# Optimization experiments

Measured on AMD Instinct MI355X. Metric: run time of the kernel, lower is better.

The kernel has to match this reference:

```python
import jax, jax.numpy as jnp
import numpy as np

T, C, H, E, TOPK = 8192, 1024, 4096, 8, 2
ALPHA = 0.01


def setup_inputs() -> dict:
    key = jax.random.key(0)
    ks = jax.random.split(key, 10)
    std = 0.01
    return {
        "x": jax.random.normal(ks[0], (T, C), dtype=jnp.float32),
        "gate_w": jax.random.normal(ks[1], (E, C), dtype=jnp.float32) * std,  # nn.init.normal_(std=0.01)
        "wg": jax.random.normal(ks[2], (E, C, H), dtype=jnp.float32) * 0.02,
        "wu": jax.random.normal(ks[3], (E, C, H), dtype=jnp.float32) * 0.02,
        "wd": jax.random.normal(ks[4], (E, H, C), dtype=jnp.float32) * 0.02,
        "swg": jax.random.normal(ks[5], (C, H), dtype=jnp.float32) * 0.02,
        "swu": jax.random.normal(ks[6], (C, H), dtype=jnp.float32) * 0.02,
        "swd": jax.random.normal(ks[7], (H, C), dtype=jnp.float32) * 0.02,
        "shared_scale": jnp.ones((1,), dtype=jnp.float32) * 0.5,
    }


def _swiglu(h, g, u, d):
    # SwiGLU FFN: W_down( silu(W_gate x) * W_up x )
    return (jax.nn.silu(h @ g) * (h @ u)) @ d


def reference(x, gate_w, wg, wu, wd, swg, swu, swd, shared_scale):
    # ---- gate (top-k softmax routing) ----
    logits = x @ gate_w.T                       # [T, E]
    scores = jax.nn.softmax(logits, axis=-1)    # [T, E]
    topk_w, topk_idx = jax.lax.top_k(scores, TOPK)
    topk_w = topk_w / jnp.sum(topk_w, axis=-1, keepdims=True)

    # per-token combine weight for each expert: sum_k w_k * [idx_k == e]  -> [T, E]
    comb = jnp.zeros((x.shape[0], E), dtype=x.dtype)
    comb = comb.at[jnp.arange(x.shape[0])[:, None], topk_idx].add(topk_w)

    # ---- routed experts (dispatch-FFN-combine, expressed as masked dense combine) ----
    y = jnp.zeros_like(x)
    for e in range(E):  # fixed small expert count
        y = y + comb[:, e:e + 1] * _swiglu(x, wg[e], wu[e], wd[e])

    # ---- shared expert ----
    y = y + shared_scale * _swiglu(x, swg, swu, swd)

    # ---- load-balancing aux loss (training mode) ----
    onehot = jax.nn.one_hot(topk_idx.reshape(-1), E, dtype=x.dtype)  # [T*K, E]
    ce = onehot.mean(axis=0)
    fi = ce * E
    Pi = scores.mean(axis=0)
    aux_loss = jnp.sum(Pi * fi) * ALPHA
    return y, aux_loss
```

## Files before the change

kernel.cpp:

```cpp
#include <hip/hip_runtime.h>
#include <hip/hip_bf16.h>
#include <stdint.h>

#define T_TOK 8192
#define CDIM  1024
#define HDIM  4096
#define NEXP  8
#define TOPK_ 2
#define GT_MAX 72
#define UT_MAX 104
#define GROWS_MAX (GT_MAX * 256)

typedef __attribute__((ext_vector_type(8))) short short8;
typedef __attribute__((ext_vector_type(4))) float f32x4;

__device__ __forceinline__ void gload16(const short* g, short* l) {
  __builtin_amdgcn_global_load_lds(
      (const __attribute__((address_space(1))) unsigned int*)(g),
      (__attribute__((address_space(3))) unsigned int*)(l), 16, 0, 0);
}

__global__ __launch_bounds__(256) void gate_kernel(
    const float* __restrict__ x, const float* __restrict__ gw,
    int* __restrict__ tokinfo, float* __restrict__ tokw,
    int* __restrict__ bcnt, float* __restrict__ spart,
    __hip_bfloat16* __restrict__ xb)
{
  const int wid = threadIdx.x >> 6, lane = threadIdx.x & 63;
  const int t = blockIdx.x * 4 + wid;
  float acc[NEXP];
#pragma unroll
  for (int e = 0; e < NEXP; ++e) acc[e] = 0.f;
  const float4* xr = (const float4*)x + (size_t)t * (CDIM / 4);
  const float4* gw4 = (const float4*)gw;
  uint2* xbo = (uint2*)(xb + (size_t)t * CDIM);
#pragma unroll
  for (int i = 0; i < CDIM / 256; ++i) {
    const float4 xv = xr[lane + 64 * i];
    union { __hip_bfloat16 h[4]; uint2 u; } o;
    o.h[0] = __float2bfloat16(xv.x); o.h[1] = __float2bfloat16(xv.y);
    o.h[2] = __float2bfloat16(xv.z); o.h[3] = __float2bfloat16(xv.w);
    xbo[lane + 64 * i] = o.u;
#pragma unroll
    for (int e = 0; e < NEXP; ++e) {
      const float4 gv = gw4[e * (CDIM / 4) + lane + 64 * i];
      acc[e] += xv.x * gv.x + xv.y * gv.y + xv.z * gv.z + xv.w * gv.w;
    }
  }
#pragma unroll
  for (int off = 32; off > 0; off >>= 1) {
#pragma unroll
    for (int e = 0; e < NEXP; ++e) acc[e] += __shfl_xor(acc[e], off);
  }
  float mx = acc[0];
#pragma unroll
  for (int e = 1; e < NEXP; ++e) mx = fmaxf(mx, acc[e]);
  float p[NEXP]; float s = 0.f;
#pragma unroll
  for (int e = 0; e < NEXP; ++e) { p[e] = __expf(acc[e] - mx); s += p[e]; }
  const float inv = 1.f / s;
#pragma unroll
  for (int e = 0; e < NEXP; ++e) p[e] *= inv;
  float v0 = p[0]; int i0 = 0;
#pragma unroll
  for (int e = 1; e < NEXP; ++e) if (p[e] > v0) { v0 = p[e]; i0 = e; }
  float v1 = -1.f; int i1 = 0;
#pragma unroll
  for (int e = 0; e < NEXP; ++e) if (e != i0 && p[e] > v1) { v1 = p[e]; i1 = e; }

  __shared__ float sp[4][NEXP];
  __shared__ int   se[4][2];
  __shared__ float swt[4][2];
  if (lane == 0) {
#pragma unroll
    for (int e = 0; e < NEXP; ++e) sp[wid][e] = p[e];
    const float wn = 1.f / (v0 + v1);
    se[wid][0] = i0; se[wid][1] = i1;
    swt[wid][0] = v0 * wn; swt[wid][1] = v1 * wn;
  }
  __syncthreads();
  if (threadIdx.x == 0) {
    int cnt[NEXP];
#pragma unroll
    for (int e = 0; e < NEXP; ++e) cnt[e] = 0;
#pragma unroll
    for (int tt = 0; tt < 4; ++tt) {
      const int e0 = se[tt][0], e1 = se[tt][1];
      const int r0 = cnt[e0]++; const int r1 = cnt[e1]++;
      tokinfo[blockIdx.x * 4 + tt] = e0 | (e1 << 3) | (r0 << 6) | (r1 << 10);
      ((float2*)tokw)[blockIdx.x * 4 + tt] = make_float2(swt[tt][0], swt[tt][1]);
    }
#pragma unroll
    for (int e = 0; e < NEXP; ++e) bcnt[blockIdx.x * NEXP + e] = cnt[e];
  }
  if (threadIdx.x < NEXP)
    spart[blockIdx.x * NEXP + threadIdx.x] =
        sp[0][threadIdx.x] + sp[1][threadIdx.x] + sp[2][threadIdx.x] + sp[3][threadIdx.x];
}

__global__ __launch_bounds__(512) void scan_kernel(
    const int* __restrict__ bcnt, int* __restrict__ boff, int* __restrict__ ecnt,
    const float* __restrict__ spart, float* __restrict__ aux_out,
    int* __restrict__ pad_off, int* __restrict__ tile_map, int* __restrict__ ntiles)
{
  const int w = threadIdx.x >> 6, l = threadIdx.x & 63;
  int run = 0;
#pragma unroll 4
  for (int c = 0; c < (T_TOK / 4) / 64; ++c) {
    const int b = c * 64 + l;
    const int v = bcnt[b * NEXP + w];
    int sc = v;
#pragma unroll
    for (int off = 1; off < 64; off <<= 1) {
      const int t = __shfl_up(sc, off);
      if (l >= off) sc += t;
    }
    boff[b * NEXP + w] = run + sc - v;
    run += __shfl(sc, 63);
  }
  if (l == 0) ecnt[w] = run;
  float fs = 0.f;
  for (int c = 0; c < (T_TOK / 4) / 64; ++c) fs += spart[(c * 64 + l) * NEXP + w];
#pragma unroll
  for (int off = 32; off > 0; off >>= 1) fs += __shfl_xor(fs, off);
  __shared__ float pis[NEXP];
  __shared__ int cs[NEXP];
  if (l == 0) { pis[w] = fs; cs[w] = run; }
  __syncthreads();
  if (threadIdx.x == 0) {
    float aux = 0.f;
#pragma unroll
    for (int e = 0; e < NEXP; ++e) {
      const float Pi = pis[e] / (float)T_TOK;
      const float ce = (float)cs[e] / (float)(T_TOK * TOPK_);
      aux += Pi * ce * (float)NEXP;
    }
    aux_out[0] = aux * 0.01f;
    ecnt[8] = T_TOK;
    int acc = 0, nt = 0;
    for (int e = 0; e < NEXP; ++e) {
      pad_off[e] = acc;
      const int te = (cs[e] + 255) >> 8;
      for (int t = 0; t < te; ++t) { tile_map[nt] = e | ((t * 256) << 4); ++nt; }
      acc += te * 256;
    }
    ntiles[0] = nt;
    for (int t = 0; t < T_TOK / 256; ++t) { tile_map[nt] = 8 | ((t * 256) << 4); ++nt; }
    ntiles[1] = nt;
  }
}

__global__ __launch_bounds__(256) void scatter_kernel(
    const int* __restrict__ tokinfo, const float* __restrict__ tokw,
    const int* __restrict__ boff, const int* __restrict__ pad_off,
    int* __restrict__ grows, float* __restrict__ gww, int2* __restrict__ tokpos)
{
  const int t = blockIdx.x * 256 + threadIdx.x;
  const int info = tokinfo[t];
  const int e0 = info & 7, e1 = (info >> 3) & 7;
  const int r0 = (info >> 6) & 15, r1 = (info >> 10) & 15;
  const int b = t >> 2;
  const float2 wv = ((const float2*)tokw)[t];
  const int g0 = pad_off[e0] + boff[b * NEXP + e0] + r0;
  grows[g0] = t; gww[g0] = wv.x;
  const int g1 = pad_off[e1] + boff[b * NEXP + e1] + r1;
  grows[g1] = t; gww[g1] = wv.y;
  tokpos[t] = make_int2(g0, g1);
}

struct TD { const float* src; __hip_bfloat16* dst; int N; int nsh; int M; };
struct TB { TD d[27]; };
__global__ __launch_bounds__(256) void tbatch_kernel(TB tb)
{
  const int m = blockIdx.x >> 12;
  const int t = blockIdx.x & 4095;
  const TD td = tb.d[m];
  const int n0 = (t & ((1 << td.nsh) - 1)) << 5;
  const int m0 = (t >> td.nsh) << 5;
  __shared__ float tile[32][33];
  const int tx = threadIdx.x & 31, ty = threadIdx.x >> 5;
#pragma unroll
  for (int i = 0; i < 4; ++i)
    tile[ty + 8 * i][tx] = td.src[(size_t)(m0 + ty + 8 * i) * td.N + n0 + tx];
  __syncthreads();
#pragma unroll
  for (int i = 0; i < 4; ++i)
    td.dst[(size_t)(n0 + ty + 8 * i) * td.M + m0 + tx] = __float2bfloat16(tile[tx][ty + 8 * i]);
}

__global__ __launch_bounds__(512, 2) void gemm1_pipe_kernel(
    const __hip_bfloat16* __restrict__ Abase,
    const __hip_bfloat16* __restrict__ B0mat, const __hip_bfloat16* __restrict__ B1mat,
    __hip_bfloat16* __restrict__ midout,
    const int* __restrict__ rowlist, const int* __restrict__ ecnt,
    const int* __restrict__ tile_map, const int* __restrict__ ntiles,
    int mode, int tile_base)
{
  constexpr int K = CDIM;
  constexpr int NTL = K / 64;
  __shared__ __align__(16) short lds[65536];

  int ti = blockIdx.y + tile_base;
  if (mode == 2) ti += ntiles[0];
  const int hi = (mode == 1) ? ntiles[0] : ntiles[1];
  if (ti >= hi) return;
  const int tm = tile_map[ti];
  const int e = tm & 15, rb = tm >> 4;
  const int rows_valid = ecnt[e] - rb;
  const int gbmid = (int)blockIdx.y * 256;
  const int glist = ti * 256;

  const int t = threadIdx.x, l = t & 63, w = t >> 6;
  const int wr = w >> 2, wc = w & 3;
  const int n0h = blockIdx.x * 128;

  const int rbase = w * 8 + (l >> 3);
  const int ksrc = ((l & 7) ^ ((l >> 3) & 7)) * 8;
  const short* pA[4]; const short* pB[4];
#pragma unroll
  for (int j = 0; j < 4; ++j) {
    const int rl_ = j * 64 + rbase;
    int rg;
    if (e == 8) rg = rb + rl_;
    else { const int c = rl_ < rows_valid ? rl_ : rows_valid - 1; rg = rowlist[glist + c]; }
    pA[j] = (const short*)Abase + (size_t)rg * K + ksrc;
    const int s = (rl_ >> 4) & 1;
    const int h = n0h + (rl_ >> 5) * 16 + (rl_ & 15);
    pB[j] = (const short*)(s ? B1mat : B0mat) + (size_t)e * CDIM * HDIM + (size_t)h * K + ksrc;
  }
  const int dst0 = w * 512 + l * 8;

#define STG(tt) { const int bb_ = ((tt) & 1) * 16384; \
    gload16(pA[0] + (tt) * 64, lds + bb_ + dst0);          gload16(pB[0] + (tt) * 64, lds + 32768 + bb_ + dst0); \
    gload16(pA[1] + (tt) * 64, lds + bb_ + 4096 + dst0);   gload16(pB[1] + (tt) * 64, lds + 32768 + bb_ + 4096 + dst0); \
    gload16(pA[2] + (tt) * 64, lds + bb_ + 8192 + dst0);   gload16(pB[2] + (tt) * 64, lds + 32768 + bb_ + 8192 + dst0); \
    gload16(pA[3] + (tt) * 64, lds + bb_ + 12288 + dst0);  gload16(pB[3] + (tt) * 64, lds + 32768 + bb_ + 12288 + dst0); }

  f32x4 acc[8][4];
#pragma unroll
  for (int i = 0; i < 8; ++i)
#pragma unroll
    for (int j = 0; j < 4; ++j) acc[i][j] = (f32x4){0.f, 0.f, 0.f, 0.f};

  STG(0)
  for (int tt = 0; tt < NTL; ++tt) {
    asm volatile("s_waitcnt vmcnt(0)\n\ts_barrier" ::: "memory");
    __builtin_amdgcn_sched_barrier(0);
    if (tt + 1 < NTL) STG(tt + 1)
    const int ab = (tt & 1) * 16384, bb = 32768 + (tt & 1) * 16384;
#pragma unroll
    for (int ks = 0; ks < 2; ++ks) {
      short8 af[8], bf[4];
      const int cb = ks * 4 + (l >> 4);
      const int csw = (cb ^ (l & 7)) * 8;
#pragma unroll
      for (int mi = 0; mi < 8; ++mi)
        af[mi] = *(const short8*)(lds + ab + (wr * 128 + mi * 16 + (l & 15)) * 64 + csw);
#pragma unroll
      for (int ni = 0; ni < 4; ++ni)
        bf[ni] = *(const short8*)(lds + bb + (wc * 64 + ni * 16 + (l & 15)) * 64 + csw);
      __builtin_amdgcn_s_setprio(1);
#pragma unroll
      for (int mi = 0; mi < 8; ++mi)
#pragma unroll
        for (int ni = 0; ni < 4; ++ni)
          acc[mi][ni] = __builtin_amdgcn_mfma_f32_16x16x32_bf16(af[mi], bf[ni], acc[mi][ni], 0, 0, 0);
      __builtin_amdgcn_s_setprio(0);
    }
  }
#undef STG

  const int rl = (l >> 4) * 4, cl = l & 15;
#pragma unroll
  for (int mi = 0; mi < 8; ++mi) {
#pragma unroll
    for (int j = 0; j < 4; ++j) {
      const int rlocal = wr * 128 + mi * 16 + rl + j;
      if (rlocal < rows_valid) {
        __hip_bfloat16* mp = midout + (size_t)(gbmid + rlocal) * HDIM;
#pragma unroll
        for (int jj = 0; jj < 2; ++jj) {
          const float g = acc[mi][jj * 2][j], u = acc[mi][jj * 2 + 1][j];
          const float sv = g / (1.f + __expf(-g));
          mp[n0h + (wc * 2 + jj) * 16 + cl] = __float2bfloat16(sv * u);
        }
      }
    }
  }
}

template <int OST>
__global__ __launch_bounds__(512, 2) void gemm2_pipe_kernel(
    const __hip_bfloat16* __restrict__ mid, const __hip_bfloat16* __restrict__ wd9,
    float* __restrict__ mid2, float* __restrict__ y,
    const int* __restrict__ rowlist, const float* __restrict__ roww,
    const int* __restrict__ ecnt, const int* __restrict__ tile_map,
    const int* __restrict__ ntiles, const float* __restrict__ ssc,
    int mode, int tile_base)
{
  constexpr int K = HDIM;
  constexpr int NTL = K / 64;
  __shared__ __align__(16) short lds[49152];

  int ti = blockIdx.y + tile_base;
  if (mode == 2) ti += ntiles[0];
  const int hi = (mode == 1) ? ntiles[0] : ntiles[1];
  if (ti >= hi) return;
  const int tm = tile_map[ti];
  const int e = tm & 15, rb = tm >> 4;
  const int rows_valid = ecnt[e] - rb;
  const int gbmid = (int)blockIdx.y * 256;
  const int glist = ti * 256;

  const int t = threadIdx.x, l = t & 63, w = t >> 6;
  const int wr = w & 3, wc = w >> 2;
  const int n0 = blockIdx.x * 128;

  const int rbase = w * 8 + (l >> 3);
  const int ksrc = ((l & 7) ^ ((l >> 3) & 7)) * 8;
  const short* pA[4]; const short* pB[2];
#pragma unroll
  for (int j = 0; j < 4; ++j)
    pA[j] = (const short*)mid + (size_t)(gbmid + j * 64 + rbase) * K + ksrc;
#pragma unroll
  for (int j = 0; j < 2; ++j)
    pB[j] = (const short*)wd9 + (size_t)e * CDIM * HDIM + (size_t)(n0 + j * 64 + rbase) * K + ksrc;
  const int dst0 = w * 512 + l * 8;

#define STG2(tt) { const int ab_ = ((tt) & 1) * 16384, bb_ = 32768 + ((tt) & 1) * 8192; \
    gload16(pA[0] + (size_t)(tt) * 64, lds + ab_ + dst0); \
    gload16(pA[1] + (size_t)(tt) * 64, lds + ab_ + 4096 + dst0); \
    gload16(pA[2] + (size_t)(tt) * 64, lds + ab_ + 8192 + dst0); \
    gload16(pA[3] + (size_t)(tt) * 64, lds + ab_ + 12288 + dst0); \
    gload16(pB[0] + (size_t)(tt) * 64, lds + bb_ + dst0); \
    gload16(pB[1] + (size_t)(tt) * 64, lds + bb_ + 4096 + dst0); }

  f32x4 acc[4][4];
#pragma unroll
  for (int i = 0; i < 4; ++i)
#pragma unroll
    for (int j = 0; j < 4; ++j) acc[i][j] = (f32x4){0.f, 0.f, 0.f, 0.f};

  STG2(0)
  for (int tt = 0; tt < NTL; ++tt) {
    asm volatile("s_waitcnt vmcnt(0)\n\ts_barrier" ::: "memory");
    __builtin_amdgcn_sched_barrier(0);
    if (tt + 1 < NTL) STG2(tt + 1)
    const int ab = (tt & 1) * 16384, bb = 32768 + (tt & 1) * 8192;
#pragma unroll
    for (int ks = 0; ks < 2; ++ks) {
      short8 af[4], bf[4];
      const int cb = ks * 4 + (l >> 4);
      const int csw = (cb ^ (l & 7)) * 8;
#pragma unroll
      for (int mi = 0; mi < 4; ++mi)
        af[mi] = *(const short8*)(lds + ab + (wr * 64 + mi * 16 + (l & 15)) * 64 + csw);
#pragma unroll
      for (int ni = 0; ni < 4; ++ni)
        bf[ni] = *(const short8*)(lds + bb + (wc * 64 + ni * 16 + (l & 15)) * 64 + csw);
      __builtin_amdgcn_s_setprio(1);
#pragma unroll
      for (int mi = 0; mi < 4; ++mi)
#pragma unroll
        for (int ni = 0; ni < 4; ++ni)
          acc[mi][ni] = __builtin_amdgcn_mfma_f32_16x16x32_bf16(af[mi], bf[ni], acc[mi][ni], 0, 0, 0);
      __builtin_amdgcn_s_setprio(0);
    }
  }
#undef STG2

  const int rl = (l >> 4) * 4, cl = l & 15;
  if (OST) {
#pragma unroll
    for (int mi = 0; mi < 4; ++mi) {
#pragma unroll
      for (int j = 0; j < 4; ++j) {
        const int rlocal = wr * 64 + mi * 16 + rl + j;
        if (rlocal < rows_valid) {
          float* mp = mid2 + (size_t)(glist + rlocal) * CDIM + n0 + wc * 64 + cl;
#pragma unroll
          for (int ni = 0; ni < 4; ++ni) mp[ni * 16] = acc[mi][ni][j];
        }
      }
    }
  } else {
    const float ss = ssc[0];
#pragma unroll
    for (int mi = 0; mi < 4; ++mi) {
#pragma unroll
      for (int j = 0; j < 4; ++j) {
        const int rlocal = wr * 64 + mi * 16 + rl + j;
        if (rlocal < rows_valid) {
          int tok; float wgt;
          if (e == 8) { tok = rb + rlocal; wgt = ss; }
          else { tok = rowlist[glist + rlocal]; wgt = roww[glist + rlocal]; }
          float* yp = y + (size_t)tok * CDIM + n0 + wc * 64 + cl;
#pragma unroll
          for (int ni = 0; ni < 4; ++ni)
            unsafeAtomicAdd(yp + ni * 16, wgt * acc[mi][ni][j]);
        }
      }
    }
  }
}

__global__ __launch_bounds__(256) void combine_kernel(
    const float* __restrict__ mid2, const int* __restrict__ ntiles,
    const int2* __restrict__ tokpos, const float* __restrict__ tokw,
    const float* __restrict__ ssc, float* __restrict__ y)
{
  const int t = blockIdx.x;
  const int c = threadIdx.x * 4;
  const int dbase = ntiles[0] * 256;
  const int2 gp = tokpos[t];
  const float2 wv = ((const float2*)tokw)[t];
  const float ss = ssc[0];
  const float4 d = *(const float4*)(mid2 + (size_t)(dbase + t) * CDIM + c);
  const float4 a = *(const float4*)(mid2 + (size_t)gp.x * CDIM + c);
  const float4 b = *(const float4*)(mid2 + (size_t)gp.y * CDIM + c);
  float4 r;
  r.x = ss * d.x + wv.x * a.x + wv.y * b.x;
  r.y = ss * d.y + wv.x * a.y + wv.y * b.y;
  r.z = ss * d.z + wv.x * a.z + wv.y * b.z;
  r.w = ss * d.w + wv.x * a.w + wv.y * b.w;
  *(float4*)(y + (size_t)t * CDIM + c) = r;
}

extern "C" void kernel_launch(void* const* d_in, const int* in_sizes, int n_in,
                              void* d_out, int out_size, void* d_ws, size_t ws_size,
                              hipStream_t stream)
{
  const float* x   = (const float*)d_in[0];
  const float* gw  = (const float*)d_in[1];
  const float* wg  = (const float*)d_in[2];
  const float* wu  = (const float*)d_in[3];
  const float* wd  = (const float*)d_in[4];
  const float* swg = (const float*)d_in[5];
  const float* swu = (const float*)d_in[6];
  const float* swd = (const float*)d_in[7];
  const float* ssc = (const float*)d_in[8];
  float* y = (float*)d_out;

  auto al = [](size_t v) { return (v + 255) & ~(size_t)255; };
  char* ws = (char*)d_ws;
  size_t off = 0;
  __hip_bfloat16* xb = (__hip_bfloat16*)(ws + off); off += al((size_t)T_TOK * CDIM * 2);
  int*   tokinfo = (int*)(ws + off);   off += al((size_t)T_TOK * 4);
  float* tokw    = (float*)(ws + off); off += al((size_t)T_TOK * 8);
  int2*  tokpos  = (int2*)(ws + off);  off += al((size_t)T_TOK * 8);
  int*   bcnt    = (int*)(ws + off);   off += al((size_t)(T_TOK / 4) * NEXP * 4);
  int*   boffb   = (int*)(ws + off);   off += al((size_t)(T_TOK / 4) * NEXP * 4);
  float* spart   = (float*)(ws + off); off += al((size_t)(T_TOK / 4) * NEXP * 4);
  int*   ecnt    = (int*)(ws + off);   off += 256;
  int*   pad_off = (int*)(ws + off);   off += 256;
  int*   ntiles  = (int*)(ws + off);   off += 256;
  int*   tile_map= (int*)(ws + off);   off += al((size_t)UT_MAX * 4);
  int*   grows   = (int*)(ws + off);   off += al((size_t)GROWS_MAX * 4);
  float* gww     = (float*)(ws + off); off += al((size_t)GROWS_MAX * 4);

  const size_t WMAT = (size_t)CDIM * HDIM;
  __hip_bfloat16* wg9 = (__hip_bfloat16*)(ws + off); off += 9 * WMAT * 2;
  __hip_bfloat16* wu9 = (__hip_bfloat16*)(ws + off); off += 9 * WMAT * 2;
  __hip_bfloat16* wd9 = (__hip_bfloat16*)(ws + off); off += 9 * WMAT * 2;
  __hip_bfloat16* mid = (__hip_bfloat16*)(ws + off);
  const size_t mid_avail = (ws_size > off) ? (ws_size - off) : 0;
  const size_t TILE_B = (size_t)256 * HDIM * 2;
  const size_t MIDB   = (size_t)UT_MAX * TILE_B;
  const size_t MID2B  = (size_t)UT_MAX * 256 * CDIM * 4;

  gate_kernel<<<T_TOK / 4, 256, 0, stream>>>(x, gw, tokinfo, tokw, bcnt, spart, xb);
  scan_kernel<<<1, 512, 0, stream>>>(bcnt, boffb, ecnt, spart, y + (size_t)T_TOK * CDIM,
                                     pad_off, tile_map, ntiles);
  scatter_kernel<<<T_TOK / 256, 256, 0, stream>>>(tokinfo, tokw, boffb, pad_off,
                                                  grows, gww, tokpos);

  TB tb;
  for (int e = 0; e < 8; ++e) {
    tb.d[e]      = TD{wg + e * WMAT, wg9 + e * WMAT, HDIM, 7, CDIM};
    tb.d[8 + e]  = TD{wu + e * WMAT, wu9 + e * WMAT, HDIM, 7, CDIM};
    tb.d[16 + e] = TD{wd + e * WMAT, wd9 + e * WMAT, CDIM, 5, HDIM};
  }
  tb.d[24] = TD{swg, wg9 + 8 * WMAT, HDIM, 7, CDIM};
  tb.d[25] = TD{swu, wu9 + 8 * WMAT, HDIM, 7, CDIM};
  tb.d[26] = TD{swd, wd9 + 8 * WMAT, CDIM, 5, HDIM};
  tbatch_kernel<<<27 * 4096, 256, 0, stream>>>(tb);

  if (mid_avail >= MIDB + MID2B) {
    float* mid2 = (float*)((char*)mid + MIDB);
    gemm1_pipe_kernel<<<dim3(HDIM / 128, UT_MAX), 512, 0, stream>>>(
        xb, wg9, wu9, mid, grows, ecnt, tile_map, ntiles, 0, 0);
    gemm2_pipe_kernel<1><<<dim3(CDIM / 128, UT_MAX), 512, 0, stream>>>(
        mid, wd9, mid2, nullptr, grows, gww, ecnt, tile_map, ntiles, ssc, 0, 0);
    combine_kernel<<<T_TOK, 256, 0, stream>>>(mid2, ntiles, tokpos, tokw, ssc, y);
  } else if (mid_avail >= MIDB) {
    hipMemsetAsync(y, 0, (size_t)T_TOK * CDIM * sizeof(float), stream);
    gemm1_pipe_kernel<<<dim3(HDIM / 128, UT_MAX), 512, 0, stream>>>(
        xb, wg9, wu9, mid, grows, ecnt, tile_map, ntiles, 0, 0);
    gemm2_pipe_kernel<0><<<dim3(CDIM / 128, UT_MAX), 512, 0, stream>>>(
        mid, wd9, nullptr, y, grows, gww, ecnt, tile_map, ntiles, ssc, 0, 0);
  } else {
    hipMemsetAsync(y, 0, (size_t)T_TOK * CDIM * sizeof(float), stream);
    int CH = (int)(mid_avail / TILE_B);
    if (CH < 1) CH = 1;
    for (int c0 = 0; c0 < GT_MAX; c0 += CH) {
      const int g = (GT_MAX - c0) < CH ? (GT_MAX - c0) : CH;
      gemm1_pipe_kernel<<<dim3(HDIM / 128, g), 512, 0, stream>>>(
          xb, wg9, wu9, mid, grows, ecnt, tile_map, ntiles, 1, c0);
      gemm2_pipe_kernel<0><<<dim3(CDIM / 128, g), 512, 0, stream>>>(
          mid, wd9, nullptr, y, grows, gww, ecnt, tile_map, ntiles, ssc, 1, c0);
    }
    for (int c0 = 0; c0 < 32; c0 += CH) {
      const int g = (32 - c0) < CH ? (32 - c0) : CH;
      gemm1_pipe_kernel<<<dim3(HDIM / 128, g), 512, 0, stream>>>(
          xb, wg9, wu9, mid, grows, ecnt, tile_map, ntiles, 2, c0);
      gemm2_pipe_kernel<0><<<dim3(CDIM / 128, g), 512, 0, stream>>>(
          mid, wd9, nullptr, y, grows, gww, ecnt, tile_map, ntiles, ssc, 2, c0);
    }
  }
}
```

Measured before the change: 1.014 ms.

## Interleave LDS fragment loads, global prefetch and MFMA quadrants in both MoE GEMMs

Both expert GEMM main loops are split into sub-phases. Each phase loads a half-tile of A/B fragments from LDS, issues part of the next tile's global-to-LDS prefetch, then runs a quadrant of MFMAs, with barriers and partial vmcnt waits between phases. This spreads memory traffic across compute instead of one vmcnt(0) wait per K-step. gemm2's wave grid changes from 4x2 to 2x4 (128 rows by 32 columns per wave), and launch bounds drop from 2 to 1 block per CU to free registers. The risk is lower occupancy and extra barriers per K-tile.

```diff
diff --git a/kernel.cpp b/kernel.cpp
--- a/kernel.cpp
+++ b/kernel.cpp
@@ -19,6 +19,10 @@
       (const __attribute__((address_space(1))) unsigned int*)(g),
       (__attribute__((address_space(3))) unsigned int*)(l), 16, 0, 0);
 }
+
+#define BAR       asm volatile("s_barrier" ::: "memory")
+#define LGKM0     do { asm volatile("s_waitcnt lgkmcnt(0)" ::: "memory"); \
+                       __builtin_amdgcn_sched_barrier(0); } while (0)
 
 __global__ __launch_bounds__(256) void gate_kernel(
     const float* __restrict__ x, const float* __restrict__ gw,
@@ -188,7 +192,7 @@
     td.dst[(size_t)(n0 + ty + 8 * i) * td.M + m0 + tx] = __float2bfloat16(tile[tx][ty + 8 * i]);
 }
 
-__global__ __launch_bounds__(512, 2) void gemm1_pipe_kernel(
+__global__ __launch_bounds__(512, 1) void gemm1_pipe_kernel(
     const __hip_bfloat16* __restrict__ Abase,
     const __hip_bfloat16* __restrict__ B0mat, const __hip_bfloat16* __restrict__ B1mat,
     __hip_bfloat16* __restrict__ midout,
@@ -230,11 +234,18 @@
   }
   const int dst0 = w * 512 + l * 8;
 
-#define STG(tt) { const int bb_ = ((tt) & 1) * 16384; \
-    gload16(pA[0] + (tt) * 64, lds + bb_ + dst0);          gload16(pB[0] + (tt) * 64, lds + 32768 + bb_ + dst0); \
-    gload16(pA[1] + (tt) * 64, lds + bb_ + 4096 + dst0);   gload16(pB[1] + (tt) * 64, lds + 32768 + bb_ + 4096 + dst0); \
-    gload16(pA[2] + (tt) * 64, lds + bb_ + 8192 + dst0);   gload16(pB[2] + (tt) * 64, lds + 32768 + bb_ + 8192 + dst0); \
-    gload16(pA[3] + (tt) * 64, lds + bb_ + 12288 + dst0);  gload16(pB[3] + (tt) * 64, lds + 32768 + bb_ + 12288 + dst0); }
+#define STG_AH(tt, h) { const int b_ = ((tt) & 1) * 16384; \
+    gload16(pA[2*(h)]   + (tt) * 64, lds + b_ + (2*(h)) * 4096   + dst0); \
+    gload16(pA[2*(h)+1] + (tt) * 64, lds + b_ + (2*(h)+1) * 4096 + dst0); }
+#define STG_BH(tt, h) { const int b_ = 32768 + ((tt) & 1) * 16384; \
+    gload16(pB[2*(h)]   + (tt) * 64, lds + b_ + (2*(h)) * 4096   + dst0); \
+    gload16(pB[2*(h)+1] + (tt) * 64, lds + b_ + (2*(h)+1) * 4096 + dst0); }
+
+  const int l15 = l & 15;
+  const int cs0 = (((l >> 4)) ^ (l & 7)) * 8;
+  const int cs1 = ((4 + (l >> 4)) ^ (l & 7)) * 8;
+  const int afb = (wr * 128 + l15) * 64;
+  const int bfb = (wc * 64 + l15) * 64;
 
   f32x4 acc[8][4];
 #pragma unroll
@@ -242,33 +253,87 @@
 #pragma unroll
     for (int j = 0; j < 4; ++j) acc[i][j] = (f32x4){0.f, 0.f, 0.f, 0.f};
 
-  STG(0)
+  short8 af[4][2], bf[4][2];
+
+  STG_AH(0, 0) STG_AH(0, 1) STG_BH(0, 0) STG_BH(0, 1)
+
   for (int tt = 0; tt < NTL; ++tt) {
-    asm volatile("s_waitcnt vmcnt(0)\n\ts_barrier" ::: "memory");
+    const int ab = (tt & 1) * 16384, bb = 32768 + (tt & 1) * 16384;
+    if (tt + 1 < NTL) {
+      STG_AH(tt + 1, 0)
+      asm volatile("s_waitcnt vmcnt(2)\n\ts_barrier" ::: "memory");
+    } else {
+      asm volatile("s_waitcnt vmcnt(0)\n\ts_barrier" ::: "memory");
+    }
     __builtin_amdgcn_sched_barrier(0);
-    if (tt + 1 < NTL) STG(tt + 1)
-    const int ab = (tt & 1) * 16384, bb = 32768 + (tt & 1) * 16384;
-#pragma unroll
-    for (int ks = 0; ks < 2; ++ks) {
-      short8 af[8], bf[4];
-      const int cb = ks * 4 + (l >> 4);
-      const int csw = (cb ^ (l & 7)) * 8;
-#pragma unroll
-      for (int mi = 0; mi < 8; ++mi)
-        af[mi] = *(const short8*)(lds + ab + (wr * 128 + mi * 16 + (l & 15)) * 64 + csw);
-#pragma unroll
-      for (int ni = 0; ni < 4; ++ni)
-        bf[ni] = *(const short8*)(lds + bb + (wc * 64 + ni * 16 + (l & 15)) * 64 + csw);
-      __builtin_amdgcn_s_setprio(1);
-#pragma unroll
-      for (int mi = 0; mi < 8; ++mi)
-#pragma unroll
-        for (int ni = 0; ni < 4; ++ni)
-          acc[mi][ni] = __builtin_amdgcn_mfma_f32_16x16x32_bf16(af[mi], bf[ni], acc[mi][ni], 0, 0, 0);
-      __builtin_amdgcn_s_setprio(0);
-    }
-  }
-#undef STG
+#pragma unroll
+    for (int mi = 0; mi < 4; ++mi) {
+      af[mi][0] = *(const short8*)(lds + ab + afb + mi * 1024 + cs0);
+      af[mi][1] = *(const short8*)(lds + ab + afb + mi * 1024 + cs1);
+    }
+#pragma unroll
+    for (int ni = 0; ni < 2; ++ni) {
+      bf[ni][0] = *(const short8*)(lds + bb + bfb + ni * 1024 + cs0);
+      bf[ni][1] = *(const short8*)(lds + bb + bfb + ni * 1024 + cs1);
+    }
+    if (tt + 1 < NTL) STG_AH(tt + 1, 1)
+    BAR; LGKM0;
+    __builtin_amdgcn_s_setprio(1);
+#pragma unroll
+    for (int ks = 0; ks < 2; ++ks)
+#pragma unroll
+      for (int mi = 0; mi < 4; ++mi)
+#pragma unroll
+        for (int ni = 0; ni < 2; ++ni)
+          acc[mi][ni] = __builtin_amdgcn_mfma_f32_16x16x32_bf16(af[mi][ks], bf[ni][ks], acc[mi][ni], 0, 0, 0);
+    __builtin_amdgcn_s_setprio(0);
+    BAR;
+#pragma unroll
+    for (int ni = 2; ni < 4; ++ni) {
+      bf[ni][0] = *(const short8*)(lds + bb + bfb + ni * 1024 + cs0);
+      bf[ni][1] = *(const short8*)(lds + bb + bfb + ni * 1024 + cs1);
+    }
+    if (tt + 1 < NTL) STG_BH(tt + 1, 0)
+    BAR; LGKM0;
+    __builtin_amdgcn_s_setprio(1);
+#pragma unroll
+    for (int ks = 0; ks < 2; ++ks)
+#pragma unroll
+      for (int mi = 0; mi < 4; ++mi)
+#pragma unroll
+        for (int ni = 0; ni < 2; ++ni)
+          acc[mi][2 + ni] = __builtin_amdgcn_mfma_f32_16x16x32_bf16(af[mi][ks], bf[2 + ni][ks], acc[mi][2 + ni], 0, 0, 0);
+    __builtin_amdgcn_s_setprio(0);
+    BAR;
+#pragma unroll
+    for (int mi = 0; mi < 4; ++mi) {
+      af[mi][0] = *(const short8*)(lds + ab + afb + 4096 + mi * 1024 + cs0);
+      af[mi][1] = *(const short8*)(lds + ab + afb + 4096 + mi * 1024 + cs1);
+    }
+    if (tt + 1 < NTL) STG_BH(tt + 1, 1)
+    BAR; LGKM0;
+    __builtin_amdgcn_s_setprio(1);
+#pragma unroll
+    for (int ks = 0; ks < 2; ++ks)
+#pragma unroll
+      for (int mi = 0; mi < 4; ++mi)
+#pragma unroll
+        for (int ni = 0; ni < 2; ++ni)
+          acc[4 + mi][ni] = __builtin_amdgcn_mfma_f32_16x16x32_bf16(af[mi][ks], bf[ni][ks], acc[4 + mi][ni], 0, 0, 0);
+    __builtin_amdgcn_s_setprio(0);
+    BAR;
+    __builtin_amdgcn_s_setprio(1);
+#pragma unroll
+    for (int ks = 0; ks < 2; ++ks)
+#pragma unroll
+      for (int mi = 0; mi < 4; ++mi)
+#pragma unroll
+        for (int ni = 0; ni < 2; ++ni)
+          acc[4 + mi][2 + ni] = __builtin_amdgcn_mfma_f32_16x16x32_bf16(af[mi][ks], bf[2 + ni][ks], acc[4 + mi][2 + ni], 0, 0, 0);
+    __builtin_amdgcn_s_setprio(0);
+  }
+#undef STG_AH
+#undef STG_BH
 
   const int rl = (l >> 4) * 4, cl = l & 15;
 #pragma unroll
@@ -290,7 +355,7 @@
 }
 
 template <int OST>
-__global__ __launch_bounds__(512, 2) void gemm2_pipe_kernel(
+__global__ __launch_bounds__(512, 1) void gemm2_pipe_kernel(
     const __hip_bfloat16* __restrict__ mid, const __hip_bfloat16* __restrict__ wd9,
     float* __restrict__ mid2, float* __restrict__ y,
     const int* __restrict__ rowlist, const float* __restrict__ roww,
@@ -313,7 +378,7 @@
   const int glist = ti * 256;
 
   const int t = threadIdx.x, l = t & 63, w = t >> 6;
-  const int wr = w & 3, wc = w >> 2;
+  const int wr = w >> 2, wc = w & 3;
   const int n0 = blockIdx.x * 128;
 
   const int rbase = w * 8 + (l >> 3);
@@ -327,77 +392,107 @@
     pB[j] = (const short*)wd9 + (size_t)e * CDIM * HDIM + (size_t)(n0 + j * 64 + rbase) * K + ksrc;
   const int dst0 = w * 512 + l * 8;
 
-#define STG2(tt) { const int ab_ = ((tt) & 1) * 16384, bb_ = 32768 + ((tt) & 1) * 8192; \
-    gload16(pA[0] + (size_t)(tt) * 64, lds + ab_ + dst0); \
-    gload16(pA[1] + (size_t)(tt) * 64, lds + ab_ + 4096 + dst0); \
-    gload16(pA[2] + (size_t)(tt) * 64, lds + ab_ + 8192 + dst0); \
-    gload16(pA[3] + (size_t)(tt) * 64, lds + ab_ + 12288 + dst0); \
-    gload16(pB[0] + (size_t)(tt) * 64, lds + bb_ + dst0); \
-    gload16(pB[1] + (size_t)(tt) * 64, lds + bb_ + 4096 + dst0); }
-
-  f32x4 acc[4][4];
-#pragma unroll
-  for (int i = 0; i < 4; ++i)
-#pragma unroll
-    for (int j = 0; j < 4; ++j) acc[i][j] = (f32x4){0.f, 0.f, 0.f, 0.f};
-
-  STG2(0)
+#define STG2_AH(tt, h) { const int b_ = ((tt) & 1) * 16384; \
+    gload16(pA[2*(h)]   + (size_t)(tt) * 64, lds + b_ + (2*(h)) * 4096   + dst0); \
+    gload16(pA[2*(h)+1] + (size_t)(tt) * 64, lds + b_ + (2*(h)+1) * 4096 + dst0); }
+#define STG2_B(tt) { const int b_ = 32768 + ((tt) & 1) * 8192; \
+    gload16(pB[0] + (size_t)(tt) * 64, lds + b_ + dst0); \
+    gload16(pB[1] + (size_t)(tt) * 64, lds + b_ + 4096 + dst0); }
+
+  const int l15 = l & 15;
+  const int cs0 = (((l >> 4)) ^ (l & 7)) * 8;
+  const int cs1 = ((4 + (l >> 4)) ^ (l & 7)) * 8;
+  const int afb = (wr * 128 + l15) * 64;
+  const int bfb = (wc * 32 + l15) * 64;
+
+  f32x4 acc[8][2];
+#pragma unroll
+  for (int i = 0; i < 8; ++i) { acc[i][0] = (f32x4){0.f,0.f,0.f,0.f}; acc[i][1] = (f32x4){0.f,0.f,0.f,0.f}; }
+
+  short8 af[4][2], bf[2][2];
+
+  STG2_AH(0, 0) STG2_AH(0, 1) STG2_B(0)
+
   for (int tt = 0; tt < NTL; ++tt) {
-    asm volatile("s_waitcnt vmcnt(0)\n\ts_barrier" ::: "memory");
+    const int ab = (tt & 1) * 16384, bb = 32768 + (tt & 1) * 8192;
+    if (tt + 1 < NTL) {
+      STG2_AH(tt + 1, 0)
+      asm volatile("s_waitcnt vmcnt(2)\n\ts_barrier" ::: "memory");
+    } else {
+      asm volatile("s_waitcnt vmcnt(0)\n\ts_barrier" ::: "memory");
+    }
     __builtin_amdgcn_sched_barrier(0);
-    if (tt + 1 < NTL) STG2(tt + 1)
-    const int ab = (tt & 1) * 16384, bb = 32768 + (tt & 1) * 8192;
-#pragma unroll
-    for (int ks = 0; ks < 2; ++ks) {
-      short8 af[4], bf[4];
-      const int cb = ks * 4 + (l >> 4);
-      const int csw = (cb ^ (l & 7)) * 8;
+#pragma unroll
+    for (int mi = 0; mi < 4; ++mi) {
+      af[mi][0] = *(const short8*)(lds + ab + afb + mi * 1024 + cs0);
+      af[mi][1] = *(const short8*)(lds + ab + afb + mi * 1024 + cs1);
+    }
+#pragma unroll
+    for (int ni = 0; ni < 2; ++ni) {
+      bf[ni][0] = *(const short8*)(lds + bb + bfb + ni * 1024 + cs0);
+      bf[ni][1] = *(const short8*)(lds + bb + bfb + ni * 1024 + cs1);
+    }
+    if (tt + 1 < NTL) STG2_AH(tt + 1, 1)
+    BAR; LGKM0;
+    __builtin_amdgcn_s_setprio(1);
+#pragma unroll
+    for (int ks = 0; ks < 2; ++ks)
 #pragma unroll
       for (int mi = 0; mi < 4; ++mi)
-        af[mi] = *(const short8*)(lds + ab + (wr * 64 + mi * 16 + (l & 15)) * 64 + csw);
-#pragma unroll
-      for (int ni = 0; ni < 4; ++ni)
-        bf[ni] = *(const short8*)(lds + bb + (wc * 64 + ni * 16 + (l & 15)) * 64 + csw);
-      __builtin_amdgcn_s_setprio(1);
+#pragma unroll
+        for (int ni = 0; ni < 2; ++ni)
+          acc[mi][ni] = __builtin_amdgcn_mfma_f32_16x16x32_bf16(af[mi][ks], bf[ni][ks], acc[mi][ni], 0, 0, 0);
+    __builtin_amdgcn_s_setprio(0);
+    BAR;
+#pragma unroll
+    for (int mi = 0; mi < 4; ++mi) {
+      af[mi][0] = *(const short8*)(lds + ab + afb + 4096 + mi * 1024 + cs0);
+      af[mi][1] = *(const short8*)(lds + ab + afb + 4096 + mi * 1024 + cs1);
+    }
+    if (tt + 1 < NTL) STG2_B(tt + 1)
+    BAR; LGKM0;
+    __builtin_amdgcn_s_setprio(1);
+#pragma unroll
+    for (int ks = 0; ks < 2; ++ks)
 #pragma unroll
       for (int mi = 0; mi < 4; ++mi)
 #pragma unroll
-        for (int ni = 0; ni < 4; ++ni)
-          acc[mi][ni] = __builtin_amdgcn_mfma_f32_16x16x32_bf16(af[mi], bf[ni], acc[mi][ni], 0, 0, 0);
-      __builtin_amdgcn_s_setprio(0);
-    }
-  }
-#undef STG2
+        for (int ni = 0; ni < 2; ++ni)
+          acc[4 + mi][ni] = __builtin_amdgcn_mfma_f32_16x16x32_bf16(af[mi][ks], bf[ni][ks], acc[4 + mi][ni], 0, 0, 0);
+    __builtin_amdgcn_s_setprio(0);
+    BAR;
+  }
+#undef STG2_AH
+#undef STG2_B
 
   const int rl = (l >> 4) * 4, cl = l & 15;
   if (OST) {
 #pragma unroll
-    for (int mi = 0; mi < 4; ++mi) {
+    for (int mi = 0; mi < 8; ++mi) {
 #pragma unroll
       for (int j = 0; j < 4; ++j) {
-        const int rlocal = wr * 64 + mi * 16 + rl + j;
+        const int rlocal = wr * 128 + mi * 16 + rl + j;
         if (rlocal < rows_valid) {
-          float* mp = mid2 + (size_t)(glist + rlocal) * CDIM + n0 + wc * 64 + cl;
-#pragma unroll
-          for (int ni = 0; ni < 4; ++ni) mp[ni * 16] = acc[mi][ni][j];
+          float* mp = mid2 + (size_t)(glist + rlocal) * CDIM + n0 + wc * 32 + cl;
+          mp[0]  = acc[mi][0][j];
+          mp[16] = acc[mi][1][j];
         }
       }
     }
   } else {
     const float ss = ssc[0];
 #pragma unroll
-    for (int mi = 0; mi < 4; ++mi) {
+    for (int mi = 0; mi < 8; ++mi) {
 #pragma unroll
       for (int j = 0; j < 4; ++j) {
-        const int rlocal = wr * 64 + mi * 16 + rl + j;
+        const int rlocal = wr * 128 + mi * 16 + rl + j;
         if (rlocal < rows_valid) {
           int tok; float wgt;
           if (e == 8) { tok = rb + rlocal; wgt = ss; }
           else { tok = rowlist[glist + rlocal]; wgt = roww[glist + rlocal]; }
-          float* yp = y + (size_t)tok * CDIM + n0 + wc * 64 + cl;
-#pragma unroll
-          for (int ni = 0; ni < 4; ++ni)
-            unsafeAtomicAdd(yp + ni * 16, wgt * acc[mi][ni][j]);
+          float* yp = y + (size_t)tok * CDIM + n0 + wc * 32 + cl;
+          unsafeAtomicAdd(yp,      wgt * acc[mi][0][j]);
+          unsafeAtomicAdd(yp + 16, wgt * acc[mi][1][j]);
         }
       }
     }
```

Result: faster. 972.3 us (-4.1%).

## Split GEMM blocks into 16 smaller-tile waves and add XCD block swizzle

Applied to the files above, without the earlier changes.

Both expert GEMM kernels now launch 1024 threads per block instead of 512, keeping the 256x128 block tile. Each wave computes a smaller sub-tile (4x4 MFMA tiles in gemm1, 4x2 in gemm2), and each thread issues fewer LDS staging loads with precomputed swizzled offsets. Block indices are remapped so that consecutive work lands on the same XCD, aiming for better L2 reuse of weights and activations. In exchange, each wave gets less operand reuse from its LDS reads. The tighter launch bounds (1024,4) may also cap VGPRs hard enough to cause spills.

```diff
diff --git a/kernel.cpp b/kernel.cpp
--- a/kernel.cpp
+++ b/kernel.cpp
@@ -18,6 +18,17 @@
   __builtin_amdgcn_global_load_lds(
       (const __attribute__((address_space(1))) unsigned int*)(g),
       (__attribute__((address_space(3))) unsigned int*)(l), 16, 0, 0);
+}
+
+__device__ __forceinline__ void xcd_swz(int& bx, int& by) {
+  const int gx = gridDim.x, gy = gridDim.y;
+  const int n = gx * gy;
+  if ((n & 7) == 0) {
+    const int id = by * gx + bx;
+    const int q = n >> 3;
+    const int wk = (id & 7) * q + (id >> 3);
+    bx = wk / gy; by = wk % gy;
+  }
 }
 
 __global__ __launch_bounds__(256) void gate_kernel(
@@ -188,7 +199,7 @@
     td.dst[(size_t)(n0 + ty + 8 * i) * td.M + m0 + tx] = __float2bfloat16(tile[tx][ty + 8 * i]);
 }
 
-__global__ __launch_bounds__(512, 2) void gemm1_pipe_kernel(
+__global__ __launch_bounds__(1024, 4) void gemm1_pipe_kernel(
     const __hip_bfloat16* __restrict__ Abase,
     const __hip_bfloat16* __restrict__ B0mat, const __hip_bfloat16* __restrict__ B1mat,
     __hip_bfloat16* __restrict__ midout,
@@ -200,26 +211,29 @@
   constexpr int NTL = K / 64;
   __shared__ __align__(16) short lds[65536];
 
-  int ti = blockIdx.y + tile_base;
+  int bx = blockIdx.x, by = blockIdx.y;
+  xcd_swz(bx, by);
+
+  int ti = by + tile_base;
   if (mode == 2) ti += ntiles[0];
   const int hi = (mode == 1) ? ntiles[0] : ntiles[1];
   if (ti >= hi) return;
   const int tm = tile_map[ti];
   const int e = tm & 15, rb = tm >> 4;
   const int rows_valid = ecnt[e] - rb;
-  const int gbmid = (int)blockIdx.y * 256;
+  const int gbmid = by * 256;
   const int glist = ti * 256;
 
   const int t = threadIdx.x, l = t & 63, w = t >> 6;
   const int wr = w >> 2, wc = w & 3;
-  const int n0h = blockIdx.x * 128;
-
-  const int rbase = w * 8 + (l >> 3);
-  const int ksrc = ((l & 7) ^ ((l >> 3) & 7)) * 8;
-  const short* pA[4]; const short* pB[4];
-#pragma unroll
-  for (int j = 0; j < 4; ++j) {
-    const int rl_ = j * 64 + rbase;
+  const int n0h = bx * 128;
+
+  const int srow = t >> 3;
+  const int ksrc = ((t & 7) ^ ((t >> 3) & 7)) * 8;
+  const short* pA[2]; const short* pB[2];
+#pragma unroll
+  for (int j = 0; j < 2; ++j) {
+    const int rl_ = j * 128 + srow;
     int rg;
     if (e == 8) rg = rb + rl_;
     else { const int c = rl_ < rows_valid ? rl_ : rows_valid - 1; rg = rowlist[glist + c]; }
@@ -228,19 +242,27 @@
     const int h = n0h + (rl_ >> 5) * 16 + (rl_ & 15);
     pB[j] = (const short*)(s ? B1mat : B0mat) + (size_t)e * CDIM * HDIM + (size_t)h * K + ksrc;
   }
-  const int dst0 = w * 512 + l * 8;
-
-#define STG(tt) { const int bb_ = ((tt) & 1) * 16384; \
-    gload16(pA[0] + (tt) * 64, lds + bb_ + dst0);          gload16(pB[0] + (tt) * 64, lds + 32768 + bb_ + dst0); \
-    gload16(pA[1] + (tt) * 64, lds + bb_ + 4096 + dst0);   gload16(pB[1] + (tt) * 64, lds + 32768 + bb_ + 4096 + dst0); \
-    gload16(pA[2] + (tt) * 64, lds + bb_ + 8192 + dst0);   gload16(pB[2] + (tt) * 64, lds + 32768 + bb_ + 8192 + dst0); \
-    gload16(pA[3] + (tt) * 64, lds + bb_ + 12288 + dst0);  gload16(pB[3] + (tt) * 64, lds + 32768 + bb_ + 12288 + dst0); }
-
-  f32x4 acc[8][4];
-#pragma unroll
-  for (int i = 0; i < 8; ++i)
+  const int dst0 = t * 8;
+
+#define STG(tt) { const int b_ = ((tt) & 1) * 16384; \
+    gload16(pA[0] + (tt) * 64, lds + b_ + dst0); \
+    gload16(pA[1] + (tt) * 64, lds + b_ + 8192 + dst0); \
+    gload16(pB[0] + (tt) * 64, lds + 32768 + b_ + dst0); \
+    gload16(pB[1] + (tt) * 64, lds + 32768 + b_ + 8192 + dst0); }
+
+  const int l15 = l & 15;
+  const int j0 = ((l >> 4) ^ (l & 7)) * 8;
+  const int j1 = ((4 + (l >> 4)) ^ (l & 7)) * 8;
+  const int arow = (wr * 64 + l15) * 64;
+  const int brow = (wc * 64 + l15) * 64;
+
+  f32x4 acc[4][4];
+#pragma unroll
+  for (int i = 0; i < 4; ++i)
 #pragma unroll
     for (int j = 0; j < 4; ++j) acc[i][j] = (f32x4){0.f, 0.f, 0.f, 0.f};
+
+  short8 af[4], bf[4];
 
   STG(0)
   for (int tt = 0; tt < NTL; ++tt) {
@@ -250,18 +272,14 @@
     const int ab = (tt & 1) * 16384, bb = 32768 + (tt & 1) * 16384;
 #pragma unroll
     for (int ks = 0; ks < 2; ++ks) {
-      short8 af[8], bf[4];
-      const int cb = ks * 4 + (l >> 4);
-      const int csw = (cb ^ (l & 7)) * 8;
-#pragma unroll
-      for (int mi = 0; mi < 8; ++mi)
-        af[mi] = *(const short8*)(lds + ab + (wr * 128 + mi * 16 + (l & 15)) * 64 + csw);
-#pragma unroll
-      for (int ni = 0; ni < 4; ++ni)
-        bf[ni] = *(const short8*)(lds + bb + (wc * 64 + ni * 16 + (l & 15)) * 64 + csw);
+      const int cj = ks ? j1 : j0;
+#pragma unroll
+      for (int mi = 0; mi < 4; ++mi) af[mi] = *(const short8*)(lds + ab + arow + mi * 1024 + cj);
+#pragma unroll
+      for (int ni = 0; ni < 4; ++ni) bf[ni] = *(const short8*)(lds + bb + brow + ni * 1024 + cj);
       __builtin_amdgcn_s_setprio(1);
 #pragma unroll
-      for (int mi = 0; mi < 8; ++mi)
+      for (int mi = 0; mi < 4; ++mi)
 #pragma unroll
         for (int ni = 0; ni < 4; ++ni)
           acc[mi][ni] = __builtin_amdgcn_mfma_f32_16x16x32_bf16(af[mi], bf[ni], acc[mi][ni], 0, 0, 0);
@@ -272,17 +290,17 @@
 
   const int rl = (l >> 4) * 4, cl = l & 15;
 #pragma unroll
-  for (int mi = 0; mi < 8; ++mi) {
+  for (int mi = 0; mi < 4; ++mi) {
 #pragma unroll
     for (int j = 0; j < 4; ++j) {
-      const int rlocal = wr * 128 + mi * 16 + rl + j;
+      const int rlocal = wr * 64 + mi * 16 + rl + j;
       if (rlocal < rows_valid) {
         __hip_bfloat16* mp = midout + (size_t)(gbmid + rlocal) * HDIM;
 #pragma unroll
         for (int jj = 0; jj < 2; ++jj) {
           const float g = acc[mi][jj * 2][j], u = acc[mi][jj * 2 + 1][j];
           const float sv = g / (1.f + __expf(-g));
-          mp[n0h + (wc * 2 + jj) * 16 + cl] = __float2bfloat16(sv * u);
+          mp[n0h + wc * 32 + jj * 16 + cl] = __float2bfloat16(sv * u);
         }
       }
     }
@@ -290,7 +308,7 @@
 }
 
 template <int OST>
-__global__ __launch_bounds__(512, 2) void gemm2_pipe_kernel(
+__global__ __launch_bounds__(1024, 4) void gemm2_pipe_kernel(
     const __hip_bfloat16* __restrict__ mid, const __hip_bfloat16* __restrict__ wd9,
     float* __restrict__ mid2, float* __restrict__ y,
     const int* __restrict__ rowlist, const float* __restrict__ roww,
@@ -302,44 +320,48 @@
   constexpr int NTL = K / 64;
   __shared__ __align__(16) short lds[49152];
 
-  int ti = blockIdx.y + tile_base;
+  int bx = blockIdx.x, by = blockIdx.y;
+  xcd_swz(bx, by);
+
+  int ti = by + tile_base;
   if (mode == 2) ti += ntiles[0];
   const int hi = (mode == 1) ? ntiles[0] : ntiles[1];
   if (ti >= hi) return;
   const int tm = tile_map[ti];
   const int e = tm & 15, rb = tm >> 4;
   const int rows_valid = ecnt[e] - rb;
-  const int gbmid = (int)blockIdx.y * 256;
+  const int gbmid = by * 256;
   const int glist = ti * 256;
 
   const int t = threadIdx.x, l = t & 63, w = t >> 6;
-  const int wr = w & 3, wc = w >> 2;
-  const int n0 = blockIdx.x * 128;
-
-  const int rbase = w * 8 + (l >> 3);
-  const int ksrc = ((l & 7) ^ ((l >> 3) & 7)) * 8;
-  const short* pA[4]; const short* pB[2];
-#pragma unroll
-  for (int j = 0; j < 4; ++j)
-    pA[j] = (const short*)mid + (size_t)(gbmid + j * 64 + rbase) * K + ksrc;
+  const int wr = w >> 2, wc = w & 3;
+  const int n0 = bx * 128;
+
+  const int srow = t >> 3;
+  const int ksrc = ((t & 7) ^ ((t >> 3) & 7)) * 8;
+  const short* pA[2];
 #pragma unroll
   for (int j = 0; j < 2; ++j)
-    pB[j] = (const short*)wd9 + (size_t)e * CDIM * HDIM + (size_t)(n0 + j * 64 + rbase) * K + ksrc;
-  const int dst0 = w * 512 + l * 8;
-
-#define STG2(tt) { const int ab_ = ((tt) & 1) * 16384, bb_ = 32768 + ((tt) & 1) * 8192; \
-    gload16(pA[0] + (size_t)(tt) * 64, lds + ab_ + dst0); \
-    gload16(pA[1] + (size_t)(tt) * 64, lds + ab_ + 4096 + dst0); \
-    gload16(pA[2] + (size_t)(tt) * 64, lds + ab_ + 8192 + dst0); \
-    gload16(pA[3] + (size_t)(tt) * 64, lds + ab_ + 12288 + dst0); \
-    gload16(pB[0] + (size_t)(tt) * 64, lds + bb_ + dst0); \
-    gload16(pB[1] + (size_t)(tt) * 64, lds + bb_ + 4096 + dst0); }
-
-  f32x4 acc[4][4];
-#pragma unroll
-  for (int i = 0; i < 4; ++i)
-#pragma unroll
-    for (int j = 0; j < 4; ++j) acc[i][j] = (f32x4){0.f, 0.f, 0.f, 0.f};
+    pA[j] = (const short*)mid + (size_t)(gbmid + j * 128 + srow) * K + ksrc;
+  const short* pB0 = (const short*)wd9 + (size_t)e * CDIM * HDIM + (size_t)(n0 + srow) * K + ksrc;
+  const int dst0 = t * 8;
+
+#define STG2(tt) { const int a_ = ((tt) & 1) * 16384, b_ = 32768 + ((tt) & 1) * 8192; \
+    gload16(pA[0] + (size_t)(tt) * 64, lds + a_ + dst0); \
+    gload16(pA[1] + (size_t)(tt) * 64, lds + a_ + 8192 + dst0); \
+    gload16(pB0   + (size_t)(tt) * 64, lds + b_ + dst0); }
+
+  const int l15 = l & 15;
+  const int j0 = ((l >> 4) ^ (l & 7)) * 8;
+  const int j1 = ((4 + (l >> 4)) ^ (l & 7)) * 8;
+  const int arow = (wr * 64 + l15) * 64;
+  const int brow = (wc * 32 + l15) * 64;
+
+  f32x4 acc[4][2];
+#pragma unroll
+  for (int i = 0; i < 4; ++i) { acc[i][0] = (f32x4){0.f,0.f,0.f,0.f}; acc[i][1] = (f32x4){0.f,0.f,0.f,0.f}; }
+
+  short8 af[4], bf[2];
 
   STG2(0)
   for (int tt = 0; tt < NTL; ++tt) {
@@ -349,21 +371,17 @@
     const int ab = (tt & 1) * 16384, bb = 32768 + (tt & 1) * 8192;
 #pragma unroll
     for (int ks = 0; ks < 2; ++ks) {
-      short8 af[4], bf[4];
-      const int cb = ks * 4 + (l >> 4);
-      const int csw = (cb ^ (l & 7)) * 8;
-#pragma unroll
-      for (int mi = 0; mi < 4; ++mi)
-        af[mi] = *(const short8*)(lds + ab + (wr * 64 + mi * 16 + (l & 15)) * 64 + csw);
-#pragma unroll
-      for (int ni = 0; ni < 4; ++ni)
-        bf[ni] = *(const short8*)(lds + bb + (wc * 64 + ni * 16 + (l & 15)) * 64 + csw);
+      const int cj = ks ? j1 : j0;
+#pragma unroll
+      for (int mi = 0; mi < 4; ++mi) af[mi] = *(const short8*)(lds + ab + arow + mi * 1024 + cj);
+      bf[0] = *(const short8*)(lds + bb + brow + cj);
+      bf[1] = *(const short8*)(lds + bb + brow + 1024 + cj);
       __builtin_amdgcn_s_setprio(1);
 #pragma unroll
-      for (int mi = 0; mi < 4; ++mi)
-#pragma unroll
-        for (int ni = 0; ni < 4; ++ni)
-          acc[mi][ni] = __builtin_amdgcn_mfma_f32_16x16x32_bf16(af[mi], bf[ni], acc[mi][ni], 0, 0, 0);
+      for (int mi = 0; mi < 4; ++mi) {
+        acc[mi][0] = __builtin_amdgcn_mfma_f32_16x16x32_bf16(af[mi], bf[0], acc[mi][0], 0, 0, 0);
+        acc[mi][1] = __builtin_amdgcn_mfma_f32_16x16x32_bf16(af[mi], bf[1], acc[mi][1], 0, 0, 0);
+      }
       __builtin_amdgcn_s_setprio(0);
     }
   }
@@ -377,9 +395,9 @@
       for (int j = 0; j < 4; ++j) {
         const int rlocal = wr * 64 + mi * 16 + rl + j;
         if (rlocal < rows_valid) {
-          float* mp = mid2 + (size_t)(glist + rlocal) * CDIM + n0 + wc * 64 + cl;
-#pragma unroll
-          for (int ni = 0; ni < 4; ++ni) mp[ni * 16] = acc[mi][ni][j];
+          float* mp = mid2 + (size_t)(glist + rlocal) * CDIM + n0 + wc * 32 + cl;
+          mp[0]  = acc[mi][0][j];
+          mp[16] = acc[mi][1][j];
         }
       }
     }
@@ -394,10 +412,9 @@
           int tok; float wgt;
           if (e == 8) { tok = rb + rlocal; wgt = ss; }
           else { tok = rowlist[glist + rlocal]; wgt = roww[glist + rlocal]; }
-          float* yp = y + (size_t)tok * CDIM + n0 + wc * 64 + cl;
-#pragma unroll
-          for (int ni = 0; ni < 4; ++ni)
-            unsafeAtomicAdd(yp + ni * 16, wgt * acc[mi][ni][j]);
+          float* yp = y + (size_t)tok * CDIM + n0 + wc * 32 + cl;
+          unsafeAtomicAdd(yp,      wgt * acc[mi][0][j]);
+          unsafeAtomicAdd(yp + 16, wgt * acc[mi][1][j]);
         }
       }
     }
@@ -487,16 +504,16 @@
 
   if (mid_avail >= MIDB + MID2B) {
     float* mid2 = (float*)((char*)mid + MIDB);
-    gemm1_pipe_kernel<<<dim3(HDIM / 128, UT_MAX), 512, 0, stream>>>(
+    gemm1_pipe_kernel<<<dim3(HDIM / 128, UT_MAX), 1024, 0, stream>>>(
         xb, wg9, wu9, mid, grows, ecnt, tile_map, ntiles, 0, 0);
-    gemm2_pipe_kernel<1><<<dim3(CDIM / 128, UT_MAX), 512, 0, stream>>>(
+    gemm2_pipe_kernel<1><<<dim3(CDIM / 128, UT_MAX), 1024, 0, stream>>>(
         mid, wd9, mid2, nullptr, grows, gww, ecnt, tile_map, ntiles, ssc, 0, 0);
     combine_kernel<<<T_TOK, 256, 0, stream>>>(mid2, ntiles, tokpos, tokw, ssc, y);
   } else if (mid_avail >= MIDB) {
     hipMemsetAsync(y, 0, (size_t)T_TOK * CDIM * sizeof(float), stream);
-    gemm1_pipe_kernel<<<dim3(HDIM / 128, UT_MAX), 512, 0, stream>>>(
+    gemm1_pipe_kernel<<<dim3(HDIM / 128, UT_MAX), 1024, 0, stream>>>(
         xb, wg9, wu9, mid, grows, ecnt, tile_map, ntiles, 0, 0);
-    gemm2_pipe_kernel<0><<<dim3(CDIM / 128, UT_MAX), 512, 0, stream>>>(
+    gemm2_pipe_kernel<0><<<dim3(CDIM / 128, UT_MAX), 1024, 0, stream>>>(
         mid, wd9, nullptr, y, grows, gww, ecnt, tile_map, ntiles, ssc, 0, 0);
   } else {
     hipMemsetAsync(y, 0, (size_t)T_TOK * CDIM * sizeof(float), stream);
@@ -504,16 +521,16 @@
     if (CH < 1) CH = 1;
     for (int c0 = 0; c0 < GT_MAX; c0 += CH) {
       const int g = (GT_MAX - c0) < CH ? (GT_MAX - c0) : CH;
-      gemm1_pipe_kernel<<<dim3(HDIM / 128, g), 512, 0, stream>>>(
+      gemm1_pipe_kernel<<<dim3(HDIM / 128, g), 1024, 0, stream>>>(
           xb, wg9, wu9, mid, grows, ecnt, tile_map, ntiles, 1, c0);
-      gemm2_pipe_kernel<0><<<dim3(CDIM / 128, g), 512, 0, stream>>>(
+      gemm2_pipe_kernel<0><<<dim3(CDIM / 128, g), 1024, 0, stream>>>(
           mid, wd9, nullptr, y, grows, gww, ecnt, tile_map, ntiles, ssc, 1, c0);
     }
     for (int c0 = 0; c0 < 32; c0 += CH) {
       const int g = (32 - c0) < CH ? (32 - c0) : CH;
-      gemm1_pipe_kernel<<<dim3(HDIM / 128, g), 512, 0, stream>>>(
+      gemm1_pipe_kernel<<<dim3(HDIM / 128, g), 1024, 0, stream>>>(
           xb, wg9, wu9, mid, grows, ecnt, tile_map, ntiles, 2, c0);
-      gemm2_pipe_kernel<0><<<dim3(CDIM / 128, g), 512, 0, stream>>>(
+      gemm2_pipe_kernel<0><<<dim3(CDIM / 128, g), 1024, 0, stream>>>(
           mid, wd9, nullptr, y, grows, gww, ecnt, tile_map, ntiles, ssc, 2, c0);
     }
   }
```

Result: faster. 984.1 us (-3.0%).
